# Kernel optimization log

Hardware: AMD Instinct MI355X
Metric: run time of the kernel (lower is better)

Reference implementation:

```python
import jax, jax.numpy as jnp
import numpy as np

KS = 3          # kernel_size
NH = 6          # num_heads
NUM_TOK = KS ** 3  # 27 neighbors per query


def setup_inputs() -> dict:
    key = jax.random.key(0)
    k1, k2, k3 = jax.random.split(key, 3)
    q = jax.random.normal(k1, (1, 40, 40, 40, 96), dtype=jnp.float32)
    k = jax.random.normal(k2, (1, 40, 40, 40, 96), dtype=jnp.float32)
    rpb = jax.random.normal(k3, (NH, KS, KS, KS), dtype=jnp.float32) * 0.02
    return {"q": q, "k": k, "rpb": rpb}


def _offsets():
    # torch.arange(-3//2+1, 3//2+1) == arange(-1, 2); meshgrid 'ij'; stacked -> [27, 3]
    r = jnp.arange(-1, 2, dtype=jnp.float32)
    g = jnp.stack(jnp.meshgrid(r, r, r, indexing="ij"), axis=-1)
    return g.reshape(NUM_TOK, 3)


def reference(q, k, rpb):
    B, H, W, T, C = q.shape
    hd = C // NH
    scale = hd ** -0.5
    N = H * W * T

    # queries: [B, N, nh, hd], pre-scaled
    qh = q.reshape(B, N, NH, hd) * scale

    # zero-pad keys by 1 voxel on each spatial side (matches nnf.pad on channels-first k)
    kp = jnp.pad(jnp.transpose(k, (0, 4, 1, 2, 3)),
                 ((0, 0), (0, 0), (1, 1), (1, 1), (1, 1)))

    # 27 shifted views == torch unfold over a 3x3x3 window (i slowest, matches grid order)
    wins = [kp[:, :, i:i + H, j:j + W, l:l + T]
            for i in range(KS) for j in range(KS) for l in range(KS)]
    Kw = jnp.stack(wins, axis=2)                 # [B, C, 27, H, W, T]
    Kw = Kw.reshape(B, NH, hd, NUM_TOK, N)        # [B, nh, hd, 27, N]

    # attention logits over the 27-token neighborhood
    attn = jnp.einsum("bnhd,bhdkn->bnhk", qh, Kw)  # [B, N, nh, 27]
    attn = attn + rpb.reshape(NH, NUM_TOK)[None, None, :, :]  # relative position bias
    attn = jax.nn.softmax(attn, axis=-1)

    # expected displacement: weighted sum of integer offsets -> [B, N, nh, 3]
    x = jnp.einsum("bnhk,kc->bnhc", attn, _offsets())
    x = x.reshape(B, H, W, T, NH * 3)
    return jnp.transpose(x, (0, 4, 1, 2, 3))      # [B, nh*3, H, W, T]
```

## Files before the change

### kernel.cpp

```cpp
#include <hip/hip_runtime.h>

typedef _Float16 h2 __attribute__((ext_vector_type(2)));

#define DH 40
#define DW 40
#define DT 40
#define NC 96
#define NH 6
#define HD 16
#define NTOK 27
#define NVOX (DH * DW * DT)

#define TX 8
#define TY 4
#define TZ 8
#define HX 10
#define HY 6
#define HZ 10
#define NHALO (HX * HY * HZ)
#define ROW_I4 3

#define TXN (DH / TX)
#define TYN (DW / TY)
#define TZN (DT / TZ)
#define NTILE (TXN * TYN * TZN)
#define NJOB (NTILE * NH)
#define NXCD 8
#define GRID 1504
#define PER_XCD (GRID / NXCD)

#if defined(__has_builtin)
#if __has_builtin(__builtin_amdgcn_fdot2)
#define HAVE_FDOT2 1
#endif
#endif

__device__ __forceinline__ float dot2acc(h2 a, h2 b, float c) {
#ifdef HAVE_FDOT2
    return __builtin_amdgcn_fdot2(a, b, c, false);
#else
    return c + (float)a.x * (float)b.x + (float)a.y * (float)b.y;
#endif
}

union I4H {
    int4 v;
    h2 h[4];
};

__global__ __launch_bounds__(256) void natt_disp_kernel(
    const float* __restrict__ q,
    const float* __restrict__ k,
    const float* __restrict__ rpb,
    float* __restrict__ out)
{
    __shared__ int4 s_k[NHALO * ROW_I4];
    __shared__ float s_rpb[NTOK];

    const int job = (blockIdx.x & (NXCD - 1)) * PER_XCD + (blockIdx.x >> 3);
    if (job >= NJOB) return;

    const int h    = job % NH;
    const int tile = job / NH;
    const int tz = tile % TZN;
    const int ty = (tile / TZN) % TYN;
    const int tx = tile / (TZN * TYN);
    const int x0 = tx * TX, y0 = ty * TY, z0 = tz * TZ;

    const int tid = threadIdx.x;

    if (tid < NTOK) s_rpb[tid] = rpb[h * NTOK + tid];

    #pragma unroll
    for (int it = 0; it < 5; ++it) {
        const int f = tid + it * 256;
        if (f < NHALO * 2) {
            const int n    = f >> 1;
            const int half = f & 1;
            const int hx = n / (HY * HZ);
            const int r  = n % (HY * HZ);
            const int hy = r / HZ;
            const int hz = r % HZ;
            const int gx = x0 - 1 + hx;
            const int gy = y0 - 1 + hy;
            const int gz = z0 - 1 + hz;
            I4H u;
            u.v = make_int4(0, 0, 0, 0);
            if (((unsigned)gx < DH) & ((unsigned)gy < DW) & ((unsigned)gz < DT)) {
                const float* src = k + ((size_t)((gx * DW + gy) * DT + gz)) * NC
                                     + h * HD + half * 8;
                const float4 a = *(const float4*)(src);
                const float4 b = *(const float4*)(src + 4);
                u.h[0] = h2{(_Float16)a.x, (_Float16)a.y};
                u.h[1] = h2{(_Float16)a.z, (_Float16)a.w};
                u.h[2] = h2{(_Float16)b.x, (_Float16)b.y};
                u.h[3] = h2{(_Float16)b.z, (_Float16)b.w};
            }
            s_k[n * ROW_I4 + half] = u.v;
        }
    }

    const int lz = tid & (TZ - 1);
    const int ly = (tid >> 3) & (TY - 1);
    const int lx = tid >> 5;
    const int vox = ((x0 + lx) * DW + (y0 + ly)) * DT + (z0 + lz);

    const float scale = 0.25f;
    h2 qh[8];
    {
        const float4* qv = (const float4*)(q + (size_t)vox * NC + h * HD);
        const float4 a = qv[0], b = qv[1], c = qv[2], d = qv[3];
        qh[0] = h2{(_Float16)(a.x * scale), (_Float16)(a.y * scale)};
        qh[1] = h2{(_Float16)(a.z * scale), (_Float16)(a.w * scale)};
        qh[2] = h2{(_Float16)(b.x * scale), (_Float16)(b.y * scale)};
        qh[3] = h2{(_Float16)(b.z * scale), (_Float16)(b.w * scale)};
        qh[4] = h2{(_Float16)(c.x * scale), (_Float16)(c.y * scale)};
        qh[5] = h2{(_Float16)(c.z * scale), (_Float16)(c.w * scale)};
        qh[6] = h2{(_Float16)(d.x * scale), (_Float16)(d.y * scale)};
        qh[7] = h2{(_Float16)(d.z * scale), (_Float16)(d.w * scale)};
    }

    __syncthreads();

    float logits[NTOK];
    #pragma unroll
    for (int i = 0; i < 3; ++i) {
        #pragma unroll
        for (int j = 0; j < 3; ++j) {
            const int base = ((lx + i) * HY + (ly + j)) * HZ + lz;
            #pragma unroll
            for (int l = 0; l < 3; ++l) {
                const int n = base + l;
                I4H u0, u1;
                u0.v = s_k[n * ROW_I4 + 0];
                u1.v = s_k[n * ROW_I4 + 1];
                float d = 0.0f;
                d = dot2acc(qh[0], u0.h[0], d);
                d = dot2acc(qh[1], u0.h[1], d);
                d = dot2acc(qh[2], u0.h[2], d);
                d = dot2acc(qh[3], u0.h[3], d);
                d = dot2acc(qh[4], u1.h[0], d);
                d = dot2acc(qh[5], u1.h[1], d);
                d = dot2acc(qh[6], u1.h[2], d);
                d = dot2acc(qh[7], u1.h[3], d);
                logits[(i * 3 + j) * 3 + l] = d + s_rpb[(i * 3 + j) * 3 + l];
            }
        }
    }

    float m = logits[0];
    #pragma unroll
    for (int kk = 1; kk < NTOK; ++kk) m = fmaxf(m, logits[kk]);
    float sum = 0.0f;
    #pragma unroll
    for (int kk = 0; kk < NTOK; ++kk) {
        const float e = __expf(logits[kk] - m);
        logits[kk] = e;
        sum += e;
    }
    const float inv = 1.0f / sum;

    float sx = 0.f, sy = 0.f, sz = 0.f;
    #pragma unroll
    for (int i = 0; i < 3; ++i) {
        #pragma unroll
        for (int j = 0; j < 3; ++j) {
            #pragma unroll
            for (int l = 0; l < 3; ++l) {
                const float a = logits[(i * 3 + j) * 3 + l];
                sx += a * (float)(i - 1);
                sy += a * (float)(j - 1);
                sz += a * (float)(l - 1);
            }
        }
    }
    sx *= inv; sy *= inv; sz *= inv;

    out[((size_t)(h * 3 + 0)) * NVOX + vox] = sx;
    out[((size_t)(h * 3 + 1)) * NVOX + vox] = sy;
    out[((size_t)(h * 3 + 2)) * NVOX + vox] = sz;
}

extern "C" void kernel_launch(void* const* d_in, const int* in_sizes, int n_in,
                              void* d_out, int out_size, void* d_ws, size_t ws_size,
                              hipStream_t stream) {
    const float* q   = (const float*)d_in[0];
    const float* k   = (const float*)d_in[1];
    const float* rpb = (const float*)d_in[2];
    float* out = (float*)d_out;

    natt_disp_kernel<<<GRID, 256, 0, stream>>>(q, k, rpb, out);
}
```

Before: 22.62 us.

## Streamline halo load, fold scale into fma, tree-reduce softmax displacement

Each thread now loads a full 16-channel key row per halo voxel instead of half, so three load iterations replace five. FP16 packing uses the pkrtz intrinsic. The query scale moves into an fma on the logit, and the position bias is held in registers instead of shared memory. The softmax uses exp2 with a folded log2e and a tree max, and the displacement sums are factored into grouped partial sums with a hardware reciprocal. This cuts ALU and shared-memory instructions, at the cost of more registers and slightly different rounding (round-toward-zero, approximate rcp, scale applied after the fp16 dot product).

```diff
diff --git a/kernel.cpp b/kernel.cpp
--- a/kernel.cpp
+++ b/kernel.cpp
@@ -29,23 +29,17 @@
 #define GRID 1504
 #define PER_XCD (GRID / NXCD)
 
-#if defined(__has_builtin)
-#if __has_builtin(__builtin_amdgcn_fdot2)
-#define HAVE_FDOT2 1
-#endif
-#endif
-
 __device__ __forceinline__ float dot2acc(h2 a, h2 b, float c) {
-#ifdef HAVE_FDOT2
     return __builtin_amdgcn_fdot2(a, b, c, false);
-#else
-    return c + (float)a.x * (float)b.x + (float)a.y * (float)b.y;
-#endif
+}
+
+__device__ __forceinline__ h2 pkrtz(float a, float b) {
+    return __builtin_bit_cast(h2, __builtin_amdgcn_cvt_pkrtz(a, b));
 }
 
 union I4H {
-    int4 v;
-    h2 h[4];
+    int4 v[2];
+    h2 h[8];
 };
 
 __global__ __launch_bounds__(256) void natt_disp_kernel(
@@ -55,7 +49,6 @@
     float* __restrict__ out)
 {
     __shared__ int4 s_k[NHALO * ROW_I4];
-    __shared__ float s_rpb[NTOK];
 
     const int job = (blockIdx.x & (NXCD - 1)) * PER_XCD + (blockIdx.x >> 3);
     if (job >= NJOB) return;
@@ -69,34 +62,45 @@
 
     const int tid = threadIdx.x;
 
-    if (tid < NTOK) s_rpb[tid] = rpb[h * NTOK + tid];
-
-    #pragma unroll
-    for (int it = 0; it < 5; ++it) {
-        const int f = tid + it * 256;
-        if (f < NHALO * 2) {
-            const int n    = f >> 1;
-            const int half = f & 1;
+    float rk[NTOK];
+    {
+        const float* rb = rpb + h * NTOK;
+        #pragma unroll
+        for (int kk = 0; kk < NTOK; ++kk) rk[kk] = rb[kk];
+    }
+
+    #pragma unroll
+    for (int it = 0; it < 3; ++it) {
+        const int n = tid + it * 256;
+        if (n < NHALO) {
             const int hx = n / (HY * HZ);
-            const int r  = n % (HY * HZ);
+            const int r  = n - hx * (HY * HZ);
             const int hy = r / HZ;
-            const int hz = r % HZ;
+            const int hz = r - hy * HZ;
             const int gx = x0 - 1 + hx;
             const int gy = y0 - 1 + hy;
             const int gz = z0 - 1 + hz;
             I4H u;
-            u.v = make_int4(0, 0, 0, 0);
+            u.v[0] = make_int4(0, 0, 0, 0);
+            u.v[1] = make_int4(0, 0, 0, 0);
             if (((unsigned)gx < DH) & ((unsigned)gy < DW) & ((unsigned)gz < DT)) {
                 const float* src = k + ((size_t)((gx * DW + gy) * DT + gz)) * NC
-                                     + h * HD + half * 8;
+                                     + h * HD;
                 const float4 a = *(const float4*)(src);
                 const float4 b = *(const float4*)(src + 4);
-                u.h[0] = h2{(_Float16)a.x, (_Float16)a.y};
-                u.h[1] = h2{(_Float16)a.z, (_Float16)a.w};
-                u.h[2] = h2{(_Float16)b.x, (_Float16)b.y};
-                u.h[3] = h2{(_Float16)b.z, (_Float16)b.w};
+                const float4 c = *(const float4*)(src + 8);
+                const float4 d = *(const float4*)(src + 12);
+                u.h[0] = pkrtz(a.x, a.y);
+                u.h[1] = pkrtz(a.z, a.w);
+                u.h[2] = pkrtz(b.x, b.y);
+                u.h[3] = pkrtz(b.z, b.w);
+                u.h[4] = pkrtz(c.x, c.y);
+                u.h[5] = pkrtz(c.z, c.w);
+                u.h[6] = pkrtz(d.x, d.y);
+                u.h[7] = pkrtz(d.z, d.w);
             }
-            s_k[n * ROW_I4 + half] = u.v;
+            s_k[n * ROW_I4 + 0] = u.v[0];
+            s_k[n * ROW_I4 + 1] = u.v[1];
         }
     }
 
@@ -105,80 +109,88 @@
     const int lx = tid >> 5;
     const int vox = ((x0 + lx) * DW + (y0 + ly)) * DT + (z0 + lz);
 
-    const float scale = 0.25f;
     h2 qh[8];
     {
         const float4* qv = (const float4*)(q + (size_t)vox * NC + h * HD);
         const float4 a = qv[0], b = qv[1], c = qv[2], d = qv[3];
-        qh[0] = h2{(_Float16)(a.x * scale), (_Float16)(a.y * scale)};
-        qh[1] = h2{(_Float16)(a.z * scale), (_Float16)(a.w * scale)};
-        qh[2] = h2{(_Float16)(b.x * scale), (_Float16)(b.y * scale)};
-        qh[3] = h2{(_Float16)(b.z * scale), (_Float16)(b.w * scale)};
-        qh[4] = h2{(_Float16)(c.x * scale), (_Float16)(c.y * scale)};
-        qh[5] = h2{(_Float16)(c.z * scale), (_Float16)(c.w * scale)};
-        qh[6] = h2{(_Float16)(d.x * scale), (_Float16)(d.y * scale)};
-        qh[7] = h2{(_Float16)(d.z * scale), (_Float16)(d.w * scale)};
+        qh[0] = pkrtz(a.x, a.y);
+        qh[1] = pkrtz(a.z, a.w);
+        qh[2] = pkrtz(b.x, b.y);
+        qh[3] = pkrtz(b.z, b.w);
+        qh[4] = pkrtz(c.x, c.y);
+        qh[5] = pkrtz(c.z, c.w);
+        qh[6] = pkrtz(d.x, d.y);
+        qh[7] = pkrtz(d.z, d.w);
     }
 
     __syncthreads();
 
-    float logits[NTOK];
+    float l[NTOK];
     #pragma unroll
     for (int i = 0; i < 3; ++i) {
         #pragma unroll
         for (int j = 0; j < 3; ++j) {
             const int base = ((lx + i) * HY + (ly + j)) * HZ + lz;
             #pragma unroll
-            for (int l = 0; l < 3; ++l) {
-                const int n = base + l;
-                I4H u0, u1;
-                u0.v = s_k[n * ROW_I4 + 0];
-                u1.v = s_k[n * ROW_I4 + 1];
+            for (int ll = 0; ll < 3; ++ll) {
+                const int n = base + ll;
+                I4H u;
+                u.v[0] = s_k[n * ROW_I4 + 0];
+                u.v[1] = s_k[n * ROW_I4 + 1];
                 float d = 0.0f;
-                d = dot2acc(qh[0], u0.h[0], d);
-                d = dot2acc(qh[1], u0.h[1], d);
-                d = dot2acc(qh[2], u0.h[2], d);
-                d = dot2acc(qh[3], u0.h[3], d);
-                d = dot2acc(qh[4], u1.h[0], d);
-                d = dot2acc(qh[5], u1.h[1], d);
-                d = dot2acc(qh[6], u1.h[2], d);
-                d = dot2acc(qh[7], u1.h[3], d);
-                logits[(i * 3 + j) * 3 + l] = d + s_rpb[(i * 3 + j) * 3 + l];
+                d = dot2acc(qh[0], u.h[0], d);
+                d = dot2acc(qh[1], u.h[1], d);
+                d = dot2acc(qh[2], u.h[2], d);
+                d = dot2acc(qh[3], u.h[3], d);
+                d = dot2acc(qh[4], u.h[4], d);
+                d = dot2acc(qh[5], u.h[5], d);
+                d = dot2acc(qh[6], u.h[6], d);
+                d = dot2acc(qh[7], u.h[7], d);
+                const int kk = (i * 3 + j) * 3 + ll;
+                l[kk] = fmaf(d, 0.25f, rk[kk]);
             }
         }
     }
 
-    float m = logits[0];
-    #pragma unroll
-    for (int kk = 1; kk < NTOK; ++kk) m = fmaxf(m, logits[kk]);
-    float sum = 0.0f;
-    #pragma unroll
-    for (int kk = 0; kk < NTOK; ++kk) {
-        const float e = __expf(logits[kk] - m);
-        logits[kk] = e;
-        sum += e;
-    }
-    const float inv = 1.0f / sum;
-
-    float sx = 0.f, sy = 0.f, sz = 0.f;
-    #pragma unroll
-    for (int i = 0; i < 3; ++i) {
-        #pragma unroll
-        for (int j = 0; j < 3; ++j) {
-            #pragma unroll
-            for (int l = 0; l < 3; ++l) {
-                const float a = logits[(i * 3 + j) * 3 + l];
-                sx += a * (float)(i - 1);
-                sy += a * (float)(j - 1);
-                sz += a * (float)(l - 1);
-            }
-        }
-    }
-    sx *= inv; sy *= inv; sz *= inv;
-
-    out[((size_t)(h * 3 + 0)) * NVOX + vox] = sx;
-    out[((size_t)(h * 3 + 1)) * NVOX + vox] = sy;
-    out[((size_t)(h * 3 + 2)) * NVOX + vox] = sz;
+    float g0 = fmaxf(fmaxf(l[0],  l[1]),  l[2]);
+    float g1 = fmaxf(fmaxf(l[3],  l[4]),  l[5]);
+    float g2 = fmaxf(fmaxf(l[6],  l[7]),  l[8]);
+    float g3 = fmaxf(fmaxf(l[9],  l[10]), l[11]);
+    float g4 = fmaxf(fmaxf(l[12], l[13]), l[14]);
+    float g5 = fmaxf(fmaxf(l[15], l[16]), l[17]);
+    float g6 = fmaxf(fmaxf(l[18], l[19]), l[20]);
+    float g7 = fmaxf(fmaxf(l[21], l[22]), l[23]);
+    float g8 = fmaxf(fmaxf(l[24], l[25]), l[26]);
+    float t0 = fmaxf(fmaxf(g0, g1), g2);
+    float t1 = fmaxf(fmaxf(g3, g4), g5);
+    float t2 = fmaxf(fmaxf(g6, g7), g8);
+    const float m = fmaxf(fmaxf(t0, t1), t2);
+
+    const float LOG2E = 1.44269504f;
+    const float nm2 = -m * LOG2E;
+    float e[NTOK];
+    #pragma unroll
+    for (int kk = 0; kk < NTOK; ++kk)
+        e[kk] = exp2f(fmaf(l[kk], LOG2E, nm2));
+
+    float s[9], zp[9];
+    #pragma unroll
+    for (int g = 0; g < 9; ++g) {
+        s[g]  = (e[g * 3] + e[g * 3 + 1]) + e[g * 3 + 2];
+        zp[g] = e[g * 3 + 2] - e[g * 3];
+    }
+    const float sum = ((s[0] + s[1]) + (s[2] + s[3]))
+                    + ((s[4] + s[5]) + (s[6] + s[7])) + s[8];
+    const float szs = ((zp[0] + zp[1]) + (zp[2] + zp[3]))
+                    + ((zp[4] + zp[5]) + (zp[6] + zp[7])) + zp[8];
+    const float sxs = ((s[6] + s[7]) + s[8]) - ((s[0] + s[1]) + s[2]);
+    const float sys = ((s[2] + s[5]) + s[8]) - ((s[0] + s[3]) + s[6]);
+
+    const float inv = __builtin_amdgcn_rcpf(sum);
+
+    out[((size_t)(h * 3 + 0)) * NVOX + vox] = sxs * inv;
+    out[((size_t)(h * 3 + 1)) * NVOX + vox] = sys * inv;
+    out[((size_t)(h * 3 + 2)) * NVOX + vox] = szs * inv;
 }
 
 extern "C" void kernel_launch(void* const* d_in, const int* in_sizes, int n_in,
```

Result: faster. 22.11 us (-2.3%).
